# Performance work log

Hardware: AMD Instinct MI355X
Metric: run time of the kernel (lower is better)

## Reference

```python
import jax, jax.numpy as jnp
import numpy as np

N = 100000   # nodes
E = 1600000  # edges per view
B = 256      # graphs in batch
D = 128      # feature dim
H, C = 4, 32 # heads, per-head channels (H*C = 128)


def _seg_softmax(logits, seg, num_seg):
    # numerically stable softmax over segments (per-destination / per-graph)
    m = jax.ops.segment_max(logits, seg, num_segments=num_seg)
    e = jnp.exp(logits - m[seg])
    s = jax.ops.segment_sum(e, seg, num_segments=num_seg)
    return e / s[seg]


def _gat_conv(x, edge_index, W, att_src, att_dst, bias):
    # PyG GATConv with add_self_loops=True, concat heads
    n = x.shape[0]
    loop = jnp.arange(n, dtype=edge_index.dtype)
    src = jnp.concatenate([edge_index[0], loop])
    dst = jnp.concatenate([edge_index[1], loop])
    xh = (x @ W).reshape(n, H, C)                      # [N,H,C]
    a_src = jnp.einsum('nhc,hc->nh', xh, att_src)      # [N,H]
    a_dst = jnp.einsum('nhc,hc->nh', xh, att_dst)
    alpha = jax.nn.leaky_relu(a_src[src] + a_dst[dst], 0.2)   # [E+N,H]
    alpha = _seg_softmax(alpha, dst, n)
    msg = xh[src] * alpha[..., None]                   # [E+N,H,C]
    out = jax.ops.segment_sum(msg, dst, num_segments=n)
    return out.reshape(n, H * C) + bias


def _global_attention(h, batch, gate_W, gate_b):
    gate = (h @ gate_W + gate_b)[:, 0]                 # [N]
    a = _seg_softmax(gate, batch, B)
    return jax.ops.segment_sum(a[:, None] * h, batch, num_segments=B)  # [B,128]


def setup_inputs() -> dict:
    key = jax.random.key(0)
    ks = jax.random.split(key, 32)
    p = lambda k, shp: (jax.random.normal(k, shp, dtype=jnp.float32) * 0.05)
    inp = {
        'x': jax.random.normal(ks[0], (N, D), dtype=jnp.float32),
        'edge_index_ast': jax.random.randint(ks[1], (2, E), 0, N, dtype=jnp.int32),
        'edge_index_cfg': jax.random.randint(ks[2], (2, E), 0, N, dtype=jnp.int32),
        'edge_index_pdg': jax.random.randint(ks[3], (2, E), 0, N, dtype=jnp.int32),
        'batch': jnp.sort(jax.random.randint(ks[4], (N,), 0, B, dtype=jnp.int32)),
        'ln_g': jnp.ones((D,), jnp.float32),
        'ln_b': jnp.zeros((D,), jnp.float32),
        'proj_W': p(ks[5], (D, D)), 'proj_b': p(ks[6], (D,)),
        'W_ast': p(ks[7], (D, H * C)), 'att_src_ast': p(ks[8], (H, C)), 'att_dst_ast': p(ks[9], (H, C)), 'bias_ast': p(ks[10], (H * C,)),
        'W_cfg': p(ks[11], (D, H * C)), 'att_src_cfg': p(ks[12], (H, C)), 'att_dst_cfg': p(ks[13], (H, C)), 'bias_cfg': p(ks[14], (H * C,)),
        'W_pdg': p(ks[15], (D, H * C)), 'att_src_pdg': p(ks[16], (H, C)), 'att_dst_pdg': p(ks[17], (H, C)), 'bias_pdg': p(ks[18], (H * C,)),
        'gate_W': p(ks[19], (H * C, 1)), 'gate_b': p(ks[20], (1,)),
        'clf_W1': p(ks[21], (3 * H * C, 128)), 'clf_b1': p(ks[22], (128,)),
        'clf_W2': p(ks[23], (128, 1)), 'clf_b2': p(ks[24], (1,)),
    }
    return inp


def reference(x, edge_index_ast, edge_index_cfg, edge_index_pdg, batch,
              ln_g, ln_b, proj_W, proj_b,
              W_ast, att_src_ast, att_dst_ast, bias_ast,
              W_cfg, att_src_cfg, att_dst_cfg, bias_cfg,
              W_pdg, att_src_pdg, att_dst_pdg, bias_pdg,
              gate_W, gate_b, clf_W1, clf_b1, clf_W2, clf_b2):
    # LayerNorm + proj + LeakyReLU (dropout = eval/no-op)
    mu = jnp.mean(x, axis=-1, keepdims=True)
    var = jnp.var(x, axis=-1, keepdims=True)
    xn = (x - mu) * jax.lax.rsqrt(var + 1e-5) * ln_g + ln_b
    h0 = jax.nn.leaky_relu(xn @ proj_W + proj_b, 0.01)

    h_ast = jax.nn.elu(_gat_conv(h0, edge_index_ast, W_ast, att_src_ast, att_dst_ast, bias_ast))
    g_ast = _global_attention(h_ast, batch, gate_W, gate_b)
    h_cfg = jax.nn.elu(_gat_conv(h0, edge_index_cfg, W_cfg, att_src_cfg, att_dst_cfg, bias_cfg))
    g_cfg = _global_attention(h_cfg, batch, gate_W, gate_b)
    h_pdg = jax.nn.elu(_gat_conv(h0, edge_index_pdg, W_pdg, att_src_pdg, att_dst_pdg, bias_pdg))
    g_pdg = _global_attention(h_pdg, batch, gate_W, gate_b)

    combined = jnp.concatenate([g_ast, g_cfg, g_pdg], axis=1)  # [B, 384]
    hid = jax.nn.leaky_relu(combined @ clf_W1 + clf_b1, 0.01)
    return (hid @ clf_W2 + clf_b2).reshape(-1)                 # [B]
```

## Files before the change

### kernel.cpp

```cpp
#include <hip/hip_runtime.h>
#include <hip/hip_bf16.h>
#include <hip/hip_fp16.h>
#include <math.h>

#define NN 100000
#define EE 1600000
#define BB 256
#define NBUCK 391
#define PBLK 384
#define CH 4167
#define TOTB (3 * PBLK)
#define ROWS_PAD 100096
#define SCAP 4608
#define OBCAP (SCAP + 256)
#define LOG2E 1.442695041f
#define GEMM_BLKS 782
#define AGG_BLKS 25000
#define XH_ELEMS ((size_t)ROWS_PAD * 128)
#define A_ELEMS ((size_t)ROWS_PAD * 4)
#define HV_ELEMS ((size_t)NN * 128)

typedef short bf16x8 __attribute__((ext_vector_type(8)));
typedef float f32x4 __attribute__((ext_vector_type(4)));

__device__ __forceinline__ unsigned short f2bf(float f) {
    __hip_bfloat16 h = __float2bfloat16(f);
    return *(unsigned short*)&h;
}
__device__ __forceinline__ unsigned short f2h(float f) {
    __half h = __float2half(f);
    return *(unsigned short*)&h;
}
__device__ __forceinline__ float h2f(unsigned short u) {
    __half h = *(__half*)&u;
    return __half2float(h);
}

__global__ __launch_bounds__(256) void prep_kernel(const float* __restrict__ W0,
                                                   const float* __restrict__ W1,
                                                   const float* __restrict__ W2,
                                                   const float* __restrict__ W3,
                                                   const float* __restrict__ ln_g,
                                                   const float* __restrict__ ln_b,
                                                   unsigned short* __restrict__ WT,
                                                   float* __restrict__ c12) {
    if (blockIdx.x < 256) {
        int which = blockIdx.x >> 6;
        const float* W = which == 0 ? W0 : which == 1 ? W1 : which == 2 ? W2 : W3;
        int i = (blockIdx.x & 63) * 256 + threadIdx.x;
        int n = i >> 7, k = i & 127;
        float v = W[k * 128 + n];
        if (which == 0) v *= ln_g[k];
        WT[which * 16384 + i] = f2bf(v);
        return;
    }
    __shared__ float p1[256], p2[256];
    int t = threadIdx.x;
    int n = t & 127, kg = t >> 7;
    float c1 = 0.f, c2 = 0.f;
    for (int k = kg * 64; k < kg * 64 + 64; k++) {
        float w = W0[k * 128 + n];
        c1 = fmaf(ln_g[k], w, c1);
        c2 = fmaf(ln_b[k], w, c2);
    }
    p1[t] = c1; p2[t] = c2;
    __syncthreads();
    if (kg == 0) {
        c12[n] = p1[n] + p1[128 + n];
        c12[128 + n] = p2[n] + p2[128 + n];
    }
}


__device__ __forceinline__ void scatter_res_body(int bid, int tid,
                                                 const int* __restrict__ e0,
                                                 const int* __restrict__ e1,
                                                 const int* __restrict__ e2,
                                                 int* __restrict__ counters,
                                                 unsigned int* __restrict__ pairbuf) {
    int v = bid / PBLK, p = bid % PBLK;
    const int* ei = v == 0 ? e0 : v == 1 ? e1 : e2;
    __shared__ int hcnt[NBUCK];
    __shared__ int cur[NBUCK];
    for (int i = tid; i < NBUCK; i += 256) hcnt[i] = 0;
    __syncthreads();
    int ea = p * CH, ebnd = min(EE, ea + CH);
    int e = ea + tid;
    for (; e + 768 < ebnd; e += 1024) {
        int d0 = ei[EE + e], d1 = ei[EE + e + 256];
        int d2 = ei[EE + e + 512], d3 = ei[EE + e + 768];
        atomicAdd(&hcnt[((unsigned)d0) >> 8], 1);
        atomicAdd(&hcnt[((unsigned)d1) >> 8], 1);
        atomicAdd(&hcnt[((unsigned)d2) >> 8], 1);
        atomicAdd(&hcnt[((unsigned)d3) >> 8], 1);
    }
    for (; e < ebnd; e += 256) atomicAdd(&hcnt[((unsigned)ei[EE + e]) >> 8], 1);
    __syncthreads();
    int* gcnt = counters + v * NBUCK;
    for (int i = tid; i < NBUCK; i += 256) {
        int c = hcnt[i];
        cur[i] = c ? atomicAdd(&gcnt[i], c) : 0;
    }
    __syncthreads();
    unsigned int* pbuf = pairbuf + (size_t)v * NBUCK * SCAP;
    e = ea + tid;
    for (; e + 768 < ebnd; e += 1024) {
        unsigned s0 = (unsigned)ei[e],       d0 = (unsigned)ei[EE + e];
        unsigned s1 = (unsigned)ei[e + 256], d1 = (unsigned)ei[EE + e + 256];
        unsigned s2 = (unsigned)ei[e + 512], d2 = (unsigned)ei[EE + e + 512];
        unsigned s3 = (unsigned)ei[e + 768], d3 = (unsigned)ei[EE + e + 768];
        int p0 = atomicAdd(&cur[d0 >> 8], 1);
        int p1 = atomicAdd(&cur[d1 >> 8], 1);
        int p2 = atomicAdd(&cur[d2 >> 8], 1);
        int p3 = atomicAdd(&cur[d3 >> 8], 1);
        if (p0 < SCAP) pbuf[(size_t)(d0 >> 8) * SCAP + p0] = (s0 << 8) | (d0 & 255u);
        if (p1 < SCAP) pbuf[(size_t)(d1 >> 8) * SCAP + p1] = (s1 << 8) | (d1 & 255u);
        if (p2 < SCAP) pbuf[(size_t)(d2 >> 8) * SCAP + p2] = (s2 << 8) | (d2 & 255u);
        if (p3 < SCAP) pbuf[(size_t)(d3 >> 8) * SCAP + p3] = (s3 << 8) | (d3 & 255u);
    }
    for (; e < ebnd; e += 256) {
        unsigned s = (unsigned)ei[e], d = (unsigned)ei[EE + e];
        int pos = atomicAdd(&cur[d >> 8], 1);
        if (pos < SCAP) pbuf[(size_t)(d >> 8) * SCAP + pos] = (s << 8) | (d & 255u);
    }
}

__device__ __forceinline__ void proj_body(int nb, int tid,
                                          const float* __restrict__ X,
                                          const unsigned short* __restrict__ WT,
                                          const float* __restrict__ c12,
                                          const float* __restrict__ pb,
                                          unsigned short* __restrict__ Out) {
    int w = tid >> 6, lane = tid & 63;
    int ln = lane & 15, oct = lane >> 4;
    int row0 = nb * 128 + w * 32;

    f32x4 acc[2][8];
    #pragma unroll
    for (int i = 0; i < 2; i++)
        #pragma unroll
        for (int j = 0; j < 8; j++) acc[i][j] = (f32x4){0.f, 0.f, 0.f, 0.f};

    const float* X0 = X + (size_t)min(row0 + ln, NN - 1) * 128;
    const float* X1 = X + (size_t)min(row0 + 16 + ln, NN - 1) * 128;
    const bf16x8* Wr = (const bf16x8*)(WT + (size_t)ln * 128);

    float s0 = 0.f, q0 = 0.f, s1 = 0.f, q1 = 0.f;
    #pragma unroll
    for (int kq = 0; kq < 4; kq++) {
        int koff = kq * 4 + oct;
        float4 xa = *(const float4*)(X0 + koff * 8);
        float4 xb = *(const float4*)(X0 + koff * 8 + 4);
        float4 ya = *(const float4*)(X1 + koff * 8);
        float4 yb = *(const float4*)(X1 + koff * 8 + 4);
        s0 += (xa.x + xa.y) + (xa.z + xa.w) + (xb.x + xb.y) + (xb.z + xb.w);
        q0 += xa.x * xa.x + xa.y * xa.y + xa.z * xa.z + xa.w * xa.w
            + xb.x * xb.x + xb.y * xb.y + xb.z * xb.z + xb.w * xb.w;
        s1 += (ya.x + ya.y) + (ya.z + ya.w) + (yb.x + yb.y) + (yb.z + yb.w);
        q1 += ya.x * ya.x + ya.y * ya.y + ya.z * ya.z + ya.w * ya.w
            + yb.x * yb.x + yb.y * yb.y + yb.z * yb.z + yb.w * yb.w;
        bf16x8 a0, a1;
        a0[0] = (short)f2bf(xa.x); a0[1] = (short)f2bf(xa.y); a0[2] = (short)f2bf(xa.z); a0[3] = (short)f2bf(xa.w);
        a0[4] = (short)f2bf(xb.x); a0[5] = (short)f2bf(xb.y); a0[6] = (short)f2bf(xb.z); a0[7] = (short)f2bf(xb.w);
        a1[0] = (short)f2bf(ya.x); a1[1] = (short)f2bf(ya.y); a1[2] = (short)f2bf(ya.z); a1[3] = (short)f2bf(ya.w);
        a1[4] = (short)f2bf(yb.x); a1[5] = (short)f2bf(yb.y); a1[6] = (short)f2bf(yb.z); a1[7] = (short)f2bf(yb.w);
        #pragma unroll
        for (int ct = 0; ct < 8; ct++) {
            bf16x8 bfr = Wr[ct * 16 * 16 + koff];
            acc[0][ct] = __builtin_amdgcn_mfma_f32_16x16x32_bf16(a0, bfr, acc[0][ct], 0, 0, 0);
            acc[1][ct] = __builtin_amdgcn_mfma_f32_16x16x32_bf16(a1, bfr, acc[1][ct], 0, 0, 0);
        }
    }
    #pragma unroll
    for (int m = 16; m < 64; m <<= 1) {
        s0 += __shfl_xor(s0, m); q0 += __shfl_xor(q0, m);
        s1 += __shfl_xor(s1, m); q1 += __shfl_xor(q1, m);
    }
    float mu0 = s0 * (1.0f / 128.0f);
    float rs0 = rsqrtf(q0 * (1.0f / 128.0f) - mu0 * mu0 + 1e-5f);
    float mu1 = s1 * (1.0f / 128.0f);
    float rs1 = rsqrtf(q1 * (1.0f / 128.0f) - mu1 * mu1 + 1e-5f);

    float c1v[8], c2v[8], pbv[8];
    #pragma unroll
    for (int ct = 0; ct < 8; ct++) {
        c1v[ct] = c12[ct * 16 + ln];
        c2v[ct] = c12[128 + ct * 16 + ln];
        pbv[ct] = pb[ct * 16 + ln];
    }
    #pragma unroll
    for (int rt = 0; rt < 2; rt++) {
        #pragma unroll
        for (int r = 0; r < 4; r++) {
            int src = oct * 4 + r;
            float rs_r = __shfl(rt ? rs1 : rs0, src);
            float mu_r = __shfl(rt ? mu1 : mu0, src);
            int row = row0 + rt * 16 + oct * 4 + r;
            #pragma unroll
            for (int ct = 0; ct < 8; ct++) {
                float v = rs_r * acc[rt][ct][r] - rs_r * mu_r * c1v[ct] + c2v[ct] + pbv[ct];
                v = v > 0.f ? v : 0.01f * v;
                Out[(size_t)row * 128 + ct * 16 + ln] = f2bf(v);
            }
        }
    }
}

__device__ __forceinline__ void view_body(int nb, int tid,
                                          const unsigned short* __restrict__ h0,
                                          const unsigned short* __restrict__ WTv,
                                          const float* __restrict__ asw,
                                          const float* __restrict__ adw,
                                          unsigned short* __restrict__ Out,
                                          float* __restrict__ a_src,
                                          float* __restrict__ a_dst) {
    int w = tid >> 6, lane = tid & 63;
    int ln = lane & 15, oct = lane >> 4;
    int row0 = nb * 128 + w * 32;

    f32x4 acc[2][8];
    #pragma unroll
    for (int i = 0; i < 2; i++)
        #pragma unroll
        for (int j = 0; j < 8; j++) acc[i][j] = (f32x4){0.f, 0.f, 0.f, 0.f};

    const bf16x8* Ar0 = (const bf16x8*)(h0 + (size_t)(row0 + ln) * 128);
    const bf16x8* Ar1 = (const bf16x8*)(h0 + (size_t)(row0 + 16 + ln) * 128);
    const bf16x8* Wr  = (const bf16x8*)(WTv + (size_t)ln * 128);

    #pragma unroll
    for (int kq = 0; kq < 4; kq++) {
        int koff = kq * 4 + oct;
        bf16x8 a0 = Ar0[koff];
        bf16x8 a1 = Ar1[koff];
        #pragma unroll
        for (int ct = 0; ct < 8; ct++) {
            bf16x8 bfr = Wr[ct * 16 * 16 + koff];
            acc[0][ct] = __builtin_amdgcn_mfma_f32_16x16x32_bf16(a0, bfr, acc[0][ct], 0, 0, 0);
            acc[1][ct] = __builtin_amdgcn_mfma_f32_16x16x32_bf16(a1, bfr, acc[1][ct], 0, 0, 0);
        }
    }
    float aswv[8], adwv[8];
    #pragma unroll
    for (int ct = 0; ct < 8; ct++) { aswv[ct] = asw[ct * 16 + ln]; adwv[ct] = adw[ct * 16 + ln]; }

    #pragma unroll
    for (int rt = 0; rt < 2; rt++) {
        #pragma unroll
        for (int r = 0; r < 4; r++) {
            int row = row0 + rt * 16 + oct * 4 + r;
            float sh_[4] = {0.f, 0.f, 0.f, 0.f}, dh_[4] = {0.f, 0.f, 0.f, 0.f};
            #pragma unroll
            for (int ct = 0; ct < 8; ct++) {
                float vv = acc[rt][ct][r];
                Out[(size_t)row * 128 + ct * 16 + ln] = f2h(vv);
                sh_[ct >> 1] = fmaf(vv, aswv[ct], sh_[ct >> 1]);
                dh_[ct >> 1] = fmaf(vv, adwv[ct], dh_[ct >> 1]);
            }
            #pragma unroll
            for (int off = 1; off < 16; off <<= 1) {
                #pragma unroll
                for (int h = 0; h < 4; h++) {
                    sh_[h] += __shfl_xor(sh_[h], off);
                    dh_[h] += __shfl_xor(dh_[h], off);
                }
            }
            if (ln == 0) {
                *(float4*)(a_src + (size_t)row * 4) = make_float4(sh_[0], sh_[1], sh_[2], sh_[3]);
                *(float4*)(a_dst + (size_t)row * 4) = make_float4(dh_[0], dh_[1], dh_[2], dh_[3]);
            }
        }
    }
}

__device__ __forceinline__ void fine_body(int bid, int t,
                                          const unsigned int* __restrict__ pairbuf,
                                          const int* __restrict__ counters,
                                          int* __restrict__ deg3,
                                          int* __restrict__ start3,
                                          unsigned int* __restrict__ ebuf3) {
    int v = bid / NBUCK, b = bid - v * NBUCK;
    int cnt = min(counters[v * NBUCK + b], SCAP);
    const unsigned int* pb = pairbuf + (size_t)(v * NBUCK + b) * SCAP;
    unsigned int* eb = ebuf3 + (size_t)(v * NBUCK + b) * OBCAP;
    int obase = (v * NBUCK + b) * OBCAP;
    __shared__ int hist[256], scan[256], cur[256];
    int node = b * 256 + t;
    int valid = (node < NN) ? 1 : 0;
    hist[t] = valid;
    __syncthreads();
    {
        int i = t;
        for (; i + 768 < cnt; i += 1024) {
            unsigned v0 = pb[i], v1 = pb[i + 256], v2 = pb[i + 512], v3 = pb[i + 768];
            atomicAdd(&hist[v0 & 255u], 1);
            atomicAdd(&hist[v1 & 255u], 1);
            atomicAdd(&hist[v2 & 255u], 1);
            atomicAdd(&hist[v3 & 255u], 1);
        }
        for (; i < cnt; i += 256) atomicAdd(&hist[pb[i] & 255u], 1);
    }
    __syncthreads();
    scan[t] = hist[t];
    __syncthreads();
    for (int s = 1; s < 256; s <<= 1) {
        int u = (t >= s) ? scan[t - s] : 0;
        __syncthreads();
        scan[t] += u;
        __syncthreads();
    }
    int excl = scan[t] - hist[t];
    cur[t] = excl + valid;
    if (valid) eb[excl] = (((unsigned)node) << 8) | ((unsigned)node & 255u);
    __syncthreads();
    {
        int i = t;
        for (; i + 768 < cnt; i += 1024) {
            unsigned v0 = pb[i], v1 = pb[i + 256], v2 = pb[i + 512], v3 = pb[i + 768];
            int p0 = atomicAdd(&cur[v0 & 255u], 1);
            int p1 = atomicAdd(&cur[v1 & 255u], 1);
            int p2 = atomicAdd(&cur[v2 & 255u], 1);
            int p3 = atomicAdd(&cur[v3 & 255u], 1);
            eb[p0] = v0; eb[p1] = v1; eb[p2] = v2; eb[p3] = v3;
        }
        for (; i < cnt; i += 256) {
            unsigned int val = pb[i];
            int pos = atomicAdd(&cur[val & 255u], 1);
            eb[pos] = val;
        }
    }
    if (valid) {
        deg3[v * NN + node] = hist[t];
        start3[v * NN + node] = obase + excl;
    }
}

__device__ __forceinline__ void agg_body(int node, int tid,
                                         const unsigned short* __restrict__ xh,
                                         const int* __restrict__ start,
                                         const int* __restrict__ deg,
                                         const unsigned int* __restrict__ ebuf,
                                         const float* __restrict__ a_src,
                                         const float* __restrict__ a_dst,
                                         const float* __restrict__ bias,
                                         const float* __restrict__ gw,
                                         const float* __restrict__ gb,
                                         unsigned short* __restrict__ hvb,
                                         float* __restrict__ gexpv,
                                         float* wlds) {
    int lane = tid & 63;
    int h = lane >> 4;
    int st = start[node];
    int cnt = deg[node];
    const char* xb = (const char*)xh;
    int laneoff = lane * 4;
    float4 ad4 = *(const float4*)(a_dst + (size_t)node * 4);
    float* ww = wlds + (tid >> 6) * 260;
    const float* wr = ww + h * 65;

    float accx = 0.f, accy = 0.f, den = 0.f;
    for (int j0 = 0; j0 < cnt; j0 += 64) {
        int nj = min(64, cnt - j0);
        int src_l = 0;
        if (lane < nj) {
            src_l = (int)(ebuf[st + j0 + lane] >> 8);
            float4 as4 = *(const float4*)(a_src + (size_t)src_l * 4);
            float t0 = as4.x + ad4.x, t1 = as4.y + ad4.y;
            float t2 = as4.z + ad4.z, t3 = as4.w + ad4.w;
            t0 = fmaxf(t0, 0.f) + 0.2f * fminf(t0, 0.f);
            t1 = fmaxf(t1, 0.f) + 0.2f * fminf(t1, 0.f);
            t2 = fmaxf(t2, 0.f) + 0.2f * fminf(t2, 0.f);
            t3 = fmaxf(t3, 0.f) + 0.2f * fminf(t3, 0.f);
            ww[0 * 65 + lane] = exp2f(t0 * LOG2E);
            ww[1 * 65 + lane] = exp2f(t1 * LOG2E);
            ww[2 * 65 + lane] = exp2f(t2 * LOG2E);
            ww[3 * 65 + lane] = exp2f(t3 * LOG2E);
        }
        int jj = 0;
        for (; jj + 4 <= nj; jj += 4) {
            int s0 = __builtin_amdgcn_readlane(src_l, jj);
            int s1 = __builtin_amdgcn_readlane(src_l, jj + 1);
            int s2 = __builtin_amdgcn_readlane(src_l, jj + 2);
            int s3 = __builtin_amdgcn_readlane(src_l, jj + 3);
            float w0 = wr[jj];
            float w1 = wr[jj + 1];
            float w2 = wr[jj + 2];
            float w3 = wr[jj + 3];
            __half2 x0 = *(const __half2*)(xb + (((size_t)(unsigned)s0) << 8) + laneoff);
            __half2 x1 = *(const __half2*)(xb + (((size_t)(unsigned)s1) << 8) + laneoff);
            __half2 x2 = *(const __half2*)(xb + (((size_t)(unsigned)s2) << 8) + laneoff);
            __half2 x3 = *(const __half2*)(xb + (((size_t)(unsigned)s3) << 8) + laneoff);
            den += w0; den += w1; den += w2; den += w3;
            accx = fmaf(__low2float(x0), w0, accx);
            accy = fmaf(__high2float(x0), w0, accy);
            accx = fmaf(__low2float(x1), w1, accx);
            accy = fmaf(__high2float(x1), w1, accy);
            accx = fmaf(__low2float(x2), w2, accx);
            accy = fmaf(__high2float(x2), w2, accy);
            accx = fmaf(__low2float(x3), w3, accx);
            accy = fmaf(__high2float(x3), w3, accy);
        }
        for (; jj < nj; jj++) {
            int s = __builtin_amdgcn_readlane(src_l, jj);
            float w = wr[jj];
            __half2 xv = *(const __half2*)(xb + (((size_t)(unsigned)s) << 8) + laneoff);
            den += w;
            accx = fmaf(__low2float(xv), w, accx);
            accy = fmaf(__high2float(xv), w, accy);
        }
    }
    float inv = 1.0f / den;
    float2 bb = *(const float2*)(bias + lane * 2);
    float o0 = accx * inv + bb.x;
    float o1 = accy * inv + bb.y;
    o0 = o0 > 0.f ? o0 : exp2f(o0 * LOG2E) - 1.0f;
    o1 = o1 > 0.f ? o1 : exp2f(o1 * LOG2E) - 1.0f;
    unsigned int packed = (unsigned)f2h(o0) | ((unsigned)f2h(o1) << 16);
    *(unsigned int*)(hvb + (size_t)node * 128 + lane * 2) = packed;
    float2 g2 = *(const float2*)(gw + lane * 2);
    float gp = o0 * g2.x + o1 * g2.y;
    #pragma unroll
    for (int m = 1; m < 64; m <<= 1) gp += __shfl_xor(gp, m);
    if (lane == 0) gexpv[node] = exp2f((gp + gb[0]) * LOG2E);
}

__device__ __forceinline__ void pool_body(int b, int tid,
                                          const unsigned short* __restrict__ hvb,
                                          const float* __restrict__ gexpv,
                                          const int* __restrict__ batch,
                                          float* __restrict__ gout,
                                          int voff,
                                          float* sacc, float* sws) {
    int g = tid >> 7;
    int ch = tid & 127;
    int l = 0, r = NN;
    while (l < r) { int m = (l + r) >> 1; if (batch[m] < b) l = m + 1; else r = m; }
    int s0 = l;
    r = NN;
    while (l < r) { int m = (l + r) >> 1; if (batch[m] < b + 1) l = m + 1; else r = m; }
    int s1 = l;
    float acc = 0.f, wsum = 0.f;
    for (int n = s0 + g; n < s1; n += 8) {
        float w = gexpv[n];
        wsum += w;
        acc = fmaf(w, h2f(hvb[(size_t)n * 128 + ch]), acc);
    }
    sacc[g * 128 + ch] = acc;
    if (ch == 0) sws[g] = wsum;
    __syncthreads();
    if (g == 0) {
        float a = 0.f, w = 0.f;
        #pragma unroll
        for (int i = 0; i < 8; i++) { a += sacc[i * 128 + ch]; w += sws[i]; }
        gout[b * 384 + voff + ch] = (s1 > s0) ? a / w : 0.f;
    }
}

__global__ __launch_bounds__(256) void fat_scatter_proj(const int* e0, const int* e1, const int* e2,
                                                        int* counters, unsigned int* pairbuf,
                                                        const float* X, const unsigned short* WT,
                                                        const float* c12, const float* pb,
                                                        unsigned short* h0) {
    if (blockIdx.x < TOTB) scatter_res_body(blockIdx.x, threadIdx.x, e0, e1, e2, counters, pairbuf);
    else proj_body(blockIdx.x - TOTB, threadIdx.x, X, WT, c12, pb, h0);
}

__global__ __launch_bounds__(256) void fat_fine_view3(const unsigned int* pairbuf, const int* counters,
                                                      int* deg3, int* start3, unsigned int* ebuf3,
                                                      const unsigned short* h0, const unsigned short* WT,
                                                      const float* as0, const float* ad0,
                                                      const float* as1, const float* ad1,
                                                      const float* as2, const float* ad2,
                                                      unsigned short* xh3, float* a_src3, float* a_dst3) {
    if (blockIdx.x < 3 * NBUCK) {
        fine_body(blockIdx.x, threadIdx.x, pairbuf, counters, deg3, start3, ebuf3);
        return;
    }
    int t = blockIdx.x - 3 * NBUCK;
    int v = t / GEMM_BLKS;
    int nb = t - v * GEMM_BLKS;
    const float* as_ = v == 0 ? as0 : v == 1 ? as1 : as2;
    const float* ad_ = v == 0 ? ad0 : v == 1 ? ad1 : ad2;
    view_body(nb, threadIdx.x, h0, WT + (size_t)(1 + v) * 16384, as_, ad_,
              xh3 + (size_t)v * XH_ELEMS,
              a_src3 + (size_t)v * A_ELEMS, a_dst3 + (size_t)v * A_ELEMS);
}

__global__ __launch_bounds__(256) void aggregate3_kernel(const unsigned short* __restrict__ xh3,
                                                         const int* __restrict__ start3,
                                                         const int* __restrict__ deg3,
                                                         const unsigned int* __restrict__ ebuf3,
                                                         const float* __restrict__ a_src3,
                                                         const float* __restrict__ a_dst3,
                                                         const float* __restrict__ b0,
                                                         const float* __restrict__ b1,
                                                         const float* __restrict__ b2,
                                                         const float* __restrict__ gw,
                                                         const float* __restrict__ gb,
                                                         unsigned short* __restrict__ hvb3,
                                                         float* __restrict__ gexpv3) {
    __shared__ float wlds[4 * 260];
    int v = blockIdx.x / AGG_BLKS;
    int bin = blockIdx.x - v * AGG_BLKS;
    int node = (bin * 256 + threadIdx.x) >> 6;
    if (node >= NN) return;
    const float* bias = v == 0 ? b0 : v == 1 ? b1 : b2;
    agg_body(node, threadIdx.x,
             xh3 + (size_t)v * XH_ELEMS,
             start3 + v * NN, deg3 + v * NN,
             ebuf3,
             a_src3 + (size_t)v * A_ELEMS, a_dst3 + (size_t)v * A_ELEMS,
             bias, gw, gb,
             hvb3 + (size_t)v * HV_ELEMS, gexpv3 + v * NN, wlds);
}

__global__ __launch_bounds__(1024) void pool3_kernel(const unsigned short* __restrict__ hvb3,
                                                     const float* __restrict__ gexpv3,
                                                     const int* __restrict__ batch,
                                                     float* __restrict__ gout) {
    __shared__ float sacc[8 * 128];
    __shared__ float sws[8];
    int v = blockIdx.x >> 8;
    int b = blockIdx.x & 255;
    pool_body(b, threadIdx.x, hvb3 + (size_t)v * HV_ELEMS, gexpv3 + v * NN,
              batch, gout, v * 128, sacc, sws);
}

__global__ __launch_bounds__(128) void clf_kernel(const float* __restrict__ gout,
                                                  const float* __restrict__ W1,
                                                  const float* __restrict__ b1,
                                                  const float* __restrict__ W2,
                                                  const float* __restrict__ b2,
                                                  float* __restrict__ out) {
    int b = blockIdx.x;
    int j = threadIdx.x;
    float acc = b1[j];
    for (int k = 0; k < 384; k++) acc = fmaf(gout[b * 384 + k], W1[k * 128 + j], acc);
    acc = acc > 0.f ? acc : 0.01f * acc;
    float p = acc * W2[j];
    #pragma unroll
    for (int m = 1; m < 64; m <<= 1) p += __shfl_xor(p, m);
    __shared__ float sh[2];
    if ((j & 63) == 0) sh[j >> 6] = p;
    __syncthreads();
    if (j == 0) out[b] = sh[0] + sh[1] + b2[0];
}

extern "C" void kernel_launch(void* const* d_in, const int* in_sizes, int n_in,
                              void* d_out, int out_size, void* d_ws, size_t ws_size,
                              hipStream_t stream) {
    const float* x      = (const float*)d_in[0];
    const int*   ei[3]  = {(const int*)d_in[1], (const int*)d_in[2], (const int*)d_in[3]};
    const int*   batch  = (const int*)d_in[4];
    const float* ln_g   = (const float*)d_in[5];
    const float* ln_b   = (const float*)d_in[6];
    const float* proj_W = (const float*)d_in[7];
    const float* proj_b = (const float*)d_in[8];
    const float* Wv[3]  = {(const float*)d_in[9],  (const float*)d_in[13], (const float*)d_in[17]};
    const float* asv[3] = {(const float*)d_in[10], (const float*)d_in[14], (const float*)d_in[18]};
    const float* adv[3] = {(const float*)d_in[11], (const float*)d_in[15], (const float*)d_in[19]};
    const float* bv[3]  = {(const float*)d_in[12], (const float*)d_in[16], (const float*)d_in[20]};
    const float* gate_W = (const float*)d_in[21];
    const float* gate_b = (const float*)d_in[22];
    const float* clf_W1 = (const float*)d_in[23];
    const float* clf_b1 = (const float*)d_in[24];
    const float* clf_W2 = (const float*)d_in[25];
    const float* clf_b2 = (const float*)d_in[26];
    float* out = (float*)d_out;

    (void)in_sizes; (void)n_in; (void)out_size; (void)ws_size;

    char* base = (char*)d_ws;
    size_t off = 0;
    auto nxt = [&](size_t bytes) { char* r = base + off; off += (bytes + 255) & ~(size_t)255; return r; };

    unsigned short* h0   = (unsigned short*)nxt((size_t)ROWS_PAD * 128 * 2);
    unsigned short* xh3  = (unsigned short*)nxt((size_t)3 * XH_ELEMS * 2);
    unsigned short* hvb3 = (unsigned short*)nxt((size_t)3 * HV_ELEMS * 2);
    unsigned short* WT   = (unsigned short*)nxt(4 * 16384 * 2);
    float* c12    = (float*)nxt(256 * 4);
    float* a_src3 = (float*)nxt((size_t)3 * A_ELEMS * 4);
    float* a_dst3 = (float*)nxt((size_t)3 * A_ELEMS * 4);
    float* gexpv3 = (float*)nxt((size_t)3 * NN * 4);
    float* gout   = (float*)nxt(BB * 384 * 4);
    int* counters = (int*)nxt(3 * NBUCK * 4);
    int* deg3     = (int*)nxt(3 * NN * 4);
    int* start3   = (int*)nxt(3 * NN * 4);
    unsigned int* ebuf3   = (unsigned int*)nxt((size_t)3 * NBUCK * OBCAP * 4);
    unsigned int* pairbuf = (unsigned int*)nxt((size_t)3 * NBUCK * SCAP * 4);

    hipMemsetAsync(counters, 0, 3 * NBUCK * 4, stream);
    prep_kernel<<<257, 256, 0, stream>>>(proj_W, Wv[0], Wv[1], Wv[2], ln_g, ln_b, WT, c12);
    fat_scatter_proj<<<TOTB + GEMM_BLKS, 256, 0, stream>>>(ei[0], ei[1], ei[2], counters, pairbuf,
                                                           x, WT, c12, proj_b, h0);
    fat_fine_view3<<<3 * NBUCK + 3 * GEMM_BLKS, 256, 0, stream>>>(
        pairbuf, counters, deg3, start3, ebuf3, h0, WT,
        asv[0], adv[0], asv[1], adv[1], asv[2], adv[2],
        xh3, a_src3, a_dst3);
    aggregate3_kernel<<<3 * AGG_BLKS, 256, 0, stream>>>(xh3, start3, deg3, ebuf3,
                                                        a_src3, a_dst3,
                                                        bv[0], bv[1], bv[2],
                                                        gate_W, gate_b, hvb3, gexpv3);
    pool3_kernel<<<3 * 256, 1024, 0, stream>>>(hvb3, gexpv3, batch, gout);
    clf_kernel<<<256, 128, 0, stream>>>(gout, clf_W1, clf_b1, clf_W2, clf_b2, out);
}
```

Before: 619.5 us.

## Split aggregation wave into two half-waves with 8-byte gathers and wave-level scan

The aggregation loop now splits each 64-lane wave into two 32-lane halves that process alternate edges. Each lane gathers 8 bytes (four fp16 channels) per edge, with the source offset and weight packed together in LDS, and the two halves are combined with a cross-half shuffle at the end. The LOG2E scaling of the attention logits moves into the GEMM epilogue, which removes a multiply per edge. The fine bucket pass replaces its LDS Hillis-Steele scan, which needed many barriers, with a wave shuffle scan plus a 4-entry cross-wave prefix. The aim is fewer loads per edge, more edges in flight, and fewer barriers, at the cost of padding odd edge counts with zero-weight entries and slightly more register pressure.

```diff
diff --git a/kernel.cpp b/kernel.cpp
--- a/kernel.cpp
+++ b/kernel.cpp
@@ -242,7 +242,10 @@
     }
     float aswv[8], adwv[8];
     #pragma unroll
-    for (int ct = 0; ct < 8; ct++) { aswv[ct] = asw[ct * 16 + ln]; adwv[ct] = adw[ct * 16 + ln]; }
+    for (int ct = 0; ct < 8; ct++) {
+        aswv[ct] = asw[ct * 16 + ln] * LOG2E;
+        adwv[ct] = adw[ct * 16 + ln] * LOG2E;
+    }
 
     #pragma unroll
     for (int rt = 0; rt < 2; rt++) {
@@ -284,7 +287,8 @@
     const unsigned int* pb = pairbuf + (size_t)(v * NBUCK + b) * SCAP;
     unsigned int* eb = ebuf3 + (size_t)(v * NBUCK + b) * OBCAP;
     int obase = (v * NBUCK + b) * OBCAP;
-    __shared__ int hist[256], scan[256], cur[256];
+    __shared__ int hist[256], cur[256];
+    __shared__ int wsum[4];
     int node = b * 256 + t;
     int valid = (node < NN) ? 1 : 0;
     hist[t] = valid;
@@ -301,15 +305,20 @@
         for (; i < cnt; i += 256) atomicAdd(&hist[pb[i] & 255u], 1);
     }
     __syncthreads();
-    scan[t] = hist[t];
-    __syncthreads();
-    for (int s = 1; s < 256; s <<= 1) {
-        int u = (t >= s) ? scan[t - s] : 0;
-        __syncthreads();
-        scan[t] += u;
-        __syncthreads();
-    }
-    int excl = scan[t] - hist[t];
+    int hv = hist[t];
+    int lanev = t & 63, wv = t >> 6;
+    int incl = hv;
+    #pragma unroll
+    for (int m = 1; m < 64; m <<= 1) {
+        int u = __shfl_up(incl, m);
+        if (lanev >= m) incl += u;
+    }
+    if (lanev == 63) wsum[wv] = incl;
+    __syncthreads();
+    int prefix = 0;
+    #pragma unroll
+    for (int i = 0; i < 4; i++) prefix += (i < wv) ? wsum[i] : 0;
+    int excl = incl + prefix - hv;
     cur[t] = excl + valid;
     if (valid) eb[excl] = (((unsigned)node) << 8) | ((unsigned)node & 255u);
     __syncthreads();
@@ -330,7 +339,7 @@
         }
     }
     if (valid) {
-        deg3[v * NN + node] = hist[t];
+        deg3[v * NN + node] = hv;
         start3[v * NN + node] = obase + excl;
     }
 }
@@ -347,80 +356,88 @@
                                          const float* __restrict__ gb,
                                          unsigned short* __restrict__ hvb,
                                          float* __restrict__ gexpv,
-                                         float* wlds) {
+                                         int2* pwlds) {
     int lane = tid & 63;
-    int h = lane >> 4;
+    int half = lane >> 5;
+    int cl = lane & 31;
+    int h = cl >> 3;
+    int cl8 = cl * 8;
     int st = start[node];
     int cnt = deg[node];
     const char* xb = (const char*)xh;
-    int laneoff = lane * 4;
     float4 ad4 = *(const float4*)(a_dst + (size_t)node * 4);
-    float* ww = wlds + (tid >> 6) * 260;
-    const float* wr = ww + h * 65;
-
-    float accx = 0.f, accy = 0.f, den = 0.f;
+    int2* pww = pwlds + (tid >> 6) * 272;
+    const int2* pr = pww + h * 68 + half;
+
+    float a0 = 0.f, a1 = 0.f, a2 = 0.f, a3 = 0.f, den = 0.f;
     for (int j0 = 0; j0 < cnt; j0 += 64) {
         int nj = min(64, cnt - j0);
-        int src_l = 0;
-        if (lane < nj) {
-            src_l = (int)(ebuf[st + j0 + lane] >> 8);
-            float4 as4 = *(const float4*)(a_src + (size_t)src_l * 4);
-            float t0 = as4.x + ad4.x, t1 = as4.y + ad4.y;
-            float t2 = as4.z + ad4.z, t3 = as4.w + ad4.w;
-            t0 = fmaxf(t0, 0.f) + 0.2f * fminf(t0, 0.f);
-            t1 = fmaxf(t1, 0.f) + 0.2f * fminf(t1, 0.f);
-            t2 = fmaxf(t2, 0.f) + 0.2f * fminf(t2, 0.f);
-            t3 = fmaxf(t3, 0.f) + 0.2f * fminf(t3, 0.f);
-            ww[0 * 65 + lane] = exp2f(t0 * LOG2E);
-            ww[1 * 65 + lane] = exp2f(t1 * LOG2E);
-            ww[2 * 65 + lane] = exp2f(t2 * LOG2E);
-            ww[3 * 65 + lane] = exp2f(t3 * LOG2E);
-        }
+        {
+            int srcb = 0;
+            float w0 = 0.f, w1 = 0.f, w2 = 0.f, w3 = 0.f;
+            if (lane < nj) {
+                int src = (int)(ebuf[st + j0 + lane] >> 8);
+                srcb = src << 8;
+                float4 as4 = *(const float4*)(a_src + (size_t)src * 4);
+                float t0 = as4.x + ad4.x, t1 = as4.y + ad4.y;
+                float t2 = as4.z + ad4.z, t3 = as4.w + ad4.w;
+                t0 = fmaxf(t0, 0.f) + 0.2f * fminf(t0, 0.f);
+                t1 = fmaxf(t1, 0.f) + 0.2f * fminf(t1, 0.f);
+                t2 = fmaxf(t2, 0.f) + 0.2f * fminf(t2, 0.f);
+                t3 = fmaxf(t3, 0.f) + 0.2f * fminf(t3, 0.f);
+                w0 = exp2f(t0); w1 = exp2f(t1); w2 = exp2f(t2); w3 = exp2f(t3);
+            }
+            int2 pv;
+            pv.x = srcb;
+            pv.y = __float_as_int(w0); pww[lane] = pv;
+            pv.y = __float_as_int(w1); pww[68 + lane] = pv;
+            pv.y = __float_as_int(w2); pww[136 + lane] = pv;
+            pv.y = __float_as_int(w3); pww[204 + lane] = pv;
+        }
+        int npad = (nj + 1) & ~1;
+        #define AGG_STEP(J) { \
+            int2 pv = pr[J]; \
+            float w = __int_as_float(pv.y); \
+            uint2 xv = *(const uint2*)(xb + (unsigned)(pv.x + cl8)); \
+            __half2 u0 = *(__half2*)&xv.x; \
+            __half2 u1 = *(__half2*)&xv.y; \
+            den += w; \
+            a0 = fmaf(__low2float(u0), w, a0); \
+            a1 = fmaf(__high2float(u0), w, a1); \
+            a2 = fmaf(__low2float(u1), w, a2); \
+            a3 = fmaf(__high2float(u1), w, a3); }
         int jj = 0;
-        for (; jj + 4 <= nj; jj += 4) {
-            int s0 = __builtin_amdgcn_readlane(src_l, jj);
-            int s1 = __builtin_amdgcn_readlane(src_l, jj + 1);
-            int s2 = __builtin_amdgcn_readlane(src_l, jj + 2);
-            int s3 = __builtin_amdgcn_readlane(src_l, jj + 3);
-            float w0 = wr[jj];
-            float w1 = wr[jj + 1];
-            float w2 = wr[jj + 2];
-            float w3 = wr[jj + 3];
-            __half2 x0 = *(const __half2*)(xb + (((size_t)(unsigned)s0) << 8) + laneoff);
-            __half2 x1 = *(const __half2*)(xb + (((size_t)(unsigned)s1) << 8) + laneoff);
-            __half2 x2 = *(const __half2*)(xb + (((size_t)(unsigned)s2) << 8) + laneoff);
-            __half2 x3 = *(const __half2*)(xb + (((size_t)(unsigned)s3) << 8) + laneoff);
-            den += w0; den += w1; den += w2; den += w3;
-            accx = fmaf(__low2float(x0), w0, accx);
-            accy = fmaf(__high2float(x0), w0, accy);
-            accx = fmaf(__low2float(x1), w1, accx);
-            accy = fmaf(__high2float(x1), w1, accy);
-            accx = fmaf(__low2float(x2), w2, accx);
-            accy = fmaf(__high2float(x2), w2, accy);
-            accx = fmaf(__low2float(x3), w3, accx);
-            accy = fmaf(__high2float(x3), w3, accy);
-        }
-        for (; jj < nj; jj++) {
-            int s = __builtin_amdgcn_readlane(src_l, jj);
-            float w = wr[jj];
-            __half2 xv = *(const __half2*)(xb + (((size_t)(unsigned)s) << 8) + laneoff);
-            den += w;
-            accx = fmaf(__low2float(xv), w, accx);
-            accy = fmaf(__high2float(xv), w, accy);
-        }
-    }
+        for (; jj + 8 <= npad; jj += 8) {
+            AGG_STEP(jj) AGG_STEP(jj + 2) AGG_STEP(jj + 4) AGG_STEP(jj + 6)
+        }
+        for (; jj < npad; jj += 2) { AGG_STEP(jj) }
+        #undef AGG_STEP
+    }
+    a0 += __shfl_xor(a0, 32);
+    a1 += __shfl_xor(a1, 32);
+    a2 += __shfl_xor(a2, 32);
+    a3 += __shfl_xor(a3, 32);
+    den += __shfl_xor(den, 32);
     float inv = 1.0f / den;
-    float2 bb = *(const float2*)(bias + lane * 2);
-    float o0 = accx * inv + bb.x;
-    float o1 = accy * inv + bb.y;
+    float4 bb4 = *(const float4*)(bias + cl * 4);
+    float o0 = a0 * inv + bb4.x;
+    float o1 = a1 * inv + bb4.y;
+    float o2 = a2 * inv + bb4.z;
+    float o3 = a3 * inv + bb4.w;
     o0 = o0 > 0.f ? o0 : exp2f(o0 * LOG2E) - 1.0f;
     o1 = o1 > 0.f ? o1 : exp2f(o1 * LOG2E) - 1.0f;
-    unsigned int packed = (unsigned)f2h(o0) | ((unsigned)f2h(o1) << 16);
-    *(unsigned int*)(hvb + (size_t)node * 128 + lane * 2) = packed;
-    float2 g2 = *(const float2*)(gw + lane * 2);
-    float gp = o0 * g2.x + o1 * g2.y;
-    #pragma unroll
-    for (int m = 1; m < 64; m <<= 1) gp += __shfl_xor(gp, m);
+    o2 = o2 > 0.f ? o2 : exp2f(o2 * LOG2E) - 1.0f;
+    o3 = o3 > 0.f ? o3 : exp2f(o3 * LOG2E) - 1.0f;
+    if (half == 0) {
+        uint2 pk;
+        pk.x = (unsigned)f2h(o0) | ((unsigned)f2h(o1) << 16);
+        pk.y = (unsigned)f2h(o2) | ((unsigned)f2h(o3) << 16);
+        *(uint2*)(hvb + (size_t)node * 128 + cl * 4) = pk;
+    }
+    float4 g4 = *(const float4*)(gw + cl * 4);
+    float gp = o0 * g4.x + o1 * g4.y + o2 * g4.z + o3 * g4.w;
+    #pragma unroll
+    for (int m = 1; m < 32; m <<= 1) gp += __shfl_xor(gp, m);
     if (lane == 0) gexpv[node] = exp2f((gp + gb[0]) * LOG2E);
 }
 
@@ -499,7 +516,7 @@
                                                          const float* __restrict__ gb,
                                                          unsigned short* __restrict__ hvb3,
                                                          float* __restrict__ gexpv3) {
-    __shared__ float wlds[4 * 260];
+    __shared__ int2 pwlds[4 * 272];
     int v = blockIdx.x / AGG_BLKS;
     int bin = blockIdx.x - v * AGG_BLKS;
     int node = (bin * 256 + threadIdx.x) >> 6;
@@ -511,7 +528,7 @@
              ebuf3,
              a_src3 + (size_t)v * A_ELEMS, a_dst3 + (size_t)v * A_ELEMS,
              bias, gw, gb,
-             hvb3 + (size_t)v * HV_ELEMS, gexpv3 + v * NN, wlds);
+             hvb3 + (size_t)v * HV_ELEMS, gexpv3 + v * NN, pwlds);
 }
 
 __global__ __launch_bounds__(1024) void pool3_kernel(const unsigned short* __restrict__ hvb3,
```

Result: slower. 643.9 us (+3.9%).
